# Optimization experiments

Hardware: AMD Instinct MI355X
Metric: run time of the kernel (lower is better)

## Reference

```python
import jax, jax.numpy as jnp
import numpy as np

HIDDEN = 1024
INTER = 4096
N_EXPERTS = 8
TOP_K = 2
INIT_STD = 0.02


def setup_inputs() -> dict:
    key = jax.random.key(0)
    ks = jax.random.split(key, 6)
    x = jax.random.normal(ks[0], (2, 1024, HIDDEN), dtype=jnp.float32)
    Wg = jax.random.normal(ks[1], (N_EXPERTS, HIDDEN), dtype=jnp.float32) * INIT_STD
    # Expert MLP params, stacked over experts. W1: [E, H, I], W2: [E, I, H].
    W1 = jax.random.normal(ks[2], (N_EXPERTS, HIDDEN, INTER), dtype=jnp.float32) * INIT_STD
    b1 = jnp.zeros((N_EXPERTS, INTER), dtype=jnp.float32)
    W2 = jax.random.normal(ks[3], (N_EXPERTS, INTER, HIDDEN), dtype=jnp.float32) * INIT_STD
    b2 = jnp.zeros((N_EXPERTS, HIDDEN), dtype=jnp.float32)
    return {"x": x, "Wg": Wg, "W1": W1, "b1": b1, "W2": W2, "b2": b2}


def reference(x, Wg, W1, b1, W2, b2):
    orig_shape = x.shape
    xt = x.reshape(-1, HIDDEN)              # [T, H]
    T = xt.shape[0]

    # Gating: top-k logits -> softmax over the k selected experts.
    logits = xt @ Wg.T                      # [T, E]
    topk_logits, topk_idx = jax.lax.top_k(logits, TOP_K)   # [T, K]
    w = jax.nn.softmax(topk_logits, axis=-1)               # [T, K]

    # Scatter top-k weights into a dense [T, E] gate matrix (zeros elsewhere).
    rows = jnp.arange(T)[:, None]
    gates = jnp.zeros((T, N_EXPERTS), xt.dtype).at[rows, topk_idx].add(w)

    # Dense expert compute (mathematically identical: non-selected experts get
    # gate weight 0). Expert MLP: Linear -> GELU (exact, erf) -> Linear.
    h = jnp.einsum('th,ehi->tei', xt, W1) + b1             # [T, E, I]
    h = jax.nn.gelu(h, approximate=False)
    o = jnp.einsum('tei,eih->teh', h, W2) + b2             # [T, E, H]
    y = jnp.einsum('te,teh->th', gates, o)                 # [T, H]
    return y.reshape(orig_shape)
```

## Files before the change

### kernel.cpp

```cpp
#include <hip/hip_runtime.h>
#include <hip/hip_bf16.h>

#define HID 1024
#define INTER 4096
#define NE 8
#define NTOK 2048
#define MAXROWS 5120

typedef __attribute__((ext_vector_type(8))) short short8v;
typedef __attribute__((ext_vector_type(4))) short short4v;
typedef __attribute__((ext_vector_type(4))) float f32x4;

__device__ __forceinline__ unsigned short f2bf(float f) {
  unsigned int u = __builtin_bit_cast(unsigned int, f);
  u = (u + 0x7FFFu + ((u >> 16) & 1u)) >> 16;
  return (unsigned short)u;
}
__device__ __forceinline__ float bf2f(unsigned short s) {
  unsigned int u = ((unsigned int)s) << 16;
  return __builtin_bit_cast(float, u);
}

typedef const __attribute__((address_space(1))) unsigned int* gas_t;
typedef __attribute__((address_space(3))) unsigned int* las_t;
__device__ __forceinline__ void gld16(const unsigned short* g, unsigned short* l) {
  __builtin_amdgcn_global_load_lds((gas_t)(const void*)g, (las_t)(void*)l, 16, 0, 0);
}

__device__ __forceinline__ void tconv_tile(const float* __restrict__ in,
                                           unsigned short* __restrict__ out,
                                           int R, int C, int bx, int by, int z,
                                           float* __restrict__ t) {
  const int r0 = by * 64, c0 = bx * 64;
  const int tr = threadIdx.x / 16;
  const int tc = (threadIdx.x % 16) * 4;
  const float* ip = in + ((size_t)z * R + r0) * (size_t)C + c0;
#pragma unroll
  for (int p = 0; p < 4; ++p) {
    f32x4 v = *(const f32x4*)&ip[(size_t)(p * 16 + tr) * C + tc];
    t[(p * 16 + tr) * 65 + tc + 0] = v[0];
    t[(p * 16 + tr) * 65 + tc + 1] = v[1];
    t[(p * 16 + tr) * 65 + tc + 2] = v[2];
    t[(p * 16 + tr) * 65 + tc + 3] = v[3];
  }
  __syncthreads();
  unsigned short* op = out + ((size_t)z * C + c0) * (size_t)R + r0;
#pragma unroll
  for (int p = 0; p < 4; ++p) {
    int c = p * 16 + tr;
    unsigned int a0 = (unsigned int)f2bf(t[(tc + 0) * 65 + c]) |
                      ((unsigned int)f2bf(t[(tc + 1) * 65 + c]) << 16);
    unsigned int a1 = (unsigned int)f2bf(t[(tc + 2) * 65 + c]) |
                      ((unsigned int)f2bf(t[(tc + 3) * 65 + c]) << 16);
    uint2 val; val.x = a0; val.y = a1;
    *(uint2*)&op[(size_t)c * R + tc] = val;
  }
}

__global__ __launch_bounds__(256) void prep_kernel(const float* __restrict__ x,
                                                   const float* __restrict__ W1,
                                                   const float* __restrict__ wg,
                                                   unsigned short* __restrict__ xb,
                                                   unsigned short* __restrict__ w1t,
                                                   int* __restrict__ tok_e,
                                                   float* __restrict__ tok_w) {
  __shared__ float sh[64 * 65];
  int bid = blockIdx.x;
  if (bid < 2048) {
    size_t i = (size_t)bid * 256 + threadIdx.x;
    f32x4 v = *(const f32x4*)&x[i * 4];
    uint2 r;
    r.x = (unsigned int)f2bf(v[0]) | ((unsigned int)f2bf(v[1]) << 16);
    r.y = (unsigned int)f2bf(v[2]) | ((unsigned int)f2bf(v[3]) << 16);
    *(uint2*)&xb[i * 4] = r;
    return;
  }
  bid -= 2048;
  if (bid < 8192) {
    tconv_tile(W1, w1t, HID, INTER, bid % 64, (bid / 64) % 16, bid / 1024, sh);
    return;
  }
  bid -= 8192;
  {
    const int t = bid;
    float acc[NE];
#pragma unroll
    for (int e = 0; e < NE; ++e) acc[e] = 0.f;
    for (int k = threadIdx.x; k < HID; k += 256) {
      float xv = x[(size_t)t * HID + k];
#pragma unroll
      for (int e = 0; e < NE; ++e) acc[e] += xv * wg[e * HID + k];
    }
#pragma unroll
    for (int e = 0; e < NE; ++e) {
#pragma unroll
      for (int off = 32; off >= 1; off >>= 1) acc[e] += __shfl_xor(acc[e], off, 64);
    }
    float* red = sh;
    const int wave = threadIdx.x >> 6, lane = threadIdx.x & 63;
    if (lane == 0) {
#pragma unroll
      for (int e = 0; e < NE; ++e) red[wave * NE + e] = acc[e];
    }
    __syncthreads();
    if (threadIdx.x == 0) {
      float l[NE];
#pragma unroll
      for (int e = 0; e < NE; ++e)
        l[e] = red[0 * NE + e] + red[1 * NE + e] + red[2 * NE + e] + red[3 * NE + e];
      int i0 = 0;
#pragma unroll
      for (int e = 1; e < NE; ++e) if (l[e] > l[i0]) i0 = e;
      int i1 = -1;
#pragma unroll
      for (int e = 0; e < NE; ++e) {
        if (e == i0) continue;
        if (i1 < 0 || l[e] > l[i1]) i1 = e;
      }
      float e1 = __expf(l[i1] - l[i0]);
      float w0 = 1.f / (1.f + e1);
      tok_e[t * 2 + 0] = i0;
      tok_e[t * 2 + 1] = i1;
      tok_w[t * 2 + 0] = w0;
      tok_w[t * 2 + 1] = 1.f - w0;
    }
  }
}

__global__ __launch_bounds__(512) void routing_kernel(const int* __restrict__ tok_e,
                                                      int* __restrict__ list_tok,
                                                      int* __restrict__ tok_gslot,
                                                      int* __restrict__ offs_out) {
  __shared__ int cnts[NE];
  __shared__ int offs_s[NE + 1];
  const int e = threadIdx.x >> 6, lane = threadIdx.x & 63;
  int c = 0;
  for (int base = 0; base < NTOK; base += 64) {
    int tok = base + lane;
    int e0 = tok_e[tok * 2], e1 = tok_e[tok * 2 + 1];
    bool m = (e0 == e) || (e1 == e);
    unsigned long long mask = __ballot(m);
    c += __popcll(mask);
  }
  if (lane == 0) cnts[e] = c;
  __syncthreads();
  if (threadIdx.x == 0) {
    int o = 0;
    for (int i = 0; i < NE; ++i) { offs_s[i] = o; o += (cnts[i] + 127) & ~127; }
    offs_s[NE] = o;
    for (int i = 0; i <= NE; ++i) offs_out[i] = offs_s[i];
  }
  __syncthreads();
  const int off = offs_s[e];
  int run = 0;
  for (int base = 0; base < NTOK; base += 64) {
    int tok = base + lane;
    int e0 = tok_e[tok * 2], e1 = tok_e[tok * 2 + 1];
    bool m = (e0 == e) || (e1 == e);
    unsigned long long mask = __ballot(m);
    int pos = run + __popcll(mask & ((1ull << lane) - 1ull));
    if (m) {
      int gs = off + pos;
      list_tok[gs] = tok;
      tok_gslot[tok * 2 + ((e0 == e) ? 0 : 1)] = gs;
    }
    run += __popcll(mask);
  }
  const int cnt = cnts[e];
  const int padded = (cnt + 127) & ~127;
  for (int p = cnt + lane; p < padded; p += 64) list_tok[off + p] = 0;
}

template <int KTOT, int NTOT, bool FIRST, int NSPLIT, int TCONVN>
__global__ __launch_bounds__(256, 3) void moe_gemm(const unsigned short* __restrict__ Abase,
                                                   const unsigned short* __restrict__ Bbase,
                                                   const float* __restrict__ bias,
                                                   const int* __restrict__ list_tok,
                                                   const int* __restrict__ offs,
                                                   void* __restrict__ outp,
                                                   const float* __restrict__ W2f,
                                                   unsigned short* __restrict__ w2t) {
  constexpr int KS = KTOT / NSPLIT;
  constexpr int NT = KS / 32;
  static_assert(NT >= 8 && (NT - 2) % 6 == 0, "NT must be 6k+2");
  constexpr int nM = MAXROWS / 128;
  constexpr int nN = NTOT / 128;
  constexpr int NWG_GEMM = nN * nM * NSPLIT;
  __shared__ __align__(16) unsigned short lds[3][2][4096];

  if (TCONVN != 0 && blockIdx.x >= NWG_GEMM) {
    int t = blockIdx.x - NWG_GEMM;
    tconv_tile(W2f, w2t, INTER, HID, t % 16, (t / 16) % 64, t / 1024,
               (float*)&lds[0][0][0]);
    return;
  }

  int wg = blockIdx.x;
  wg = (wg & 7) * (NWG_GEMM >> 3) + (wg >> 3);
  const int ks = (NSPLIT > 1) ? (wg / (nM * nN)) : 0;
  const int rem = wg % (nM * nN);
  const int mt = rem % nM;
  const int nt = rem / nM;
  const int grow0 = mt * 128;
  if (grow0 >= offs[NE]) return;
  int e = 0;
#pragma unroll
  for (int i = 1; i < NE; ++i) if (grow0 >= offs[i]) e = i;
  const int n0 = nt * 128;
  const int k0 = ks * KS;

  const int tid = threadIdx.x;
  const int wave = tid >> 6, lane = tid & 63;

  const int srow = tid >> 2;
  const int skc = (((tid & 3) ^ ((srow >> 1) & 3)) * 8);
  const unsigned short* ag[2];
  const unsigned short* bg[2];
#pragma unroll
  for (int j = 0; j < 2; ++j) {
    const int row = srow + j * 64;
    size_t arow;
    if (FIRST) arow = (size_t)list_tok[grow0 + row] * KTOT;
    else       arow = (size_t)(grow0 + row) * KTOT;
    ag[j] = Abase + arow + k0 + skc;
    bg[j] = Bbase + (size_t)e * NTOT * KTOT + (size_t)(n0 + row) * KTOT + k0 + skc;
  }
  const int wbase = wave * 512;

  const int wm = wave >> 1, wn = wave & 1;
  const int fr = lane & 15;
  const int q = lane >> 4;
  int aoff[4], boff[4];
#pragma unroll
  for (int m = 0; m < 4; ++m) {
    const int row = wm * 64 + m * 16 + fr;
    aoff[m] = row * 32 + ((q ^ ((row >> 1) & 3)) * 8);
  }
#pragma unroll
  for (int n = 0; n < 4; ++n) {
    const int row = wn * 64 + n * 16 + fr;
    boff[n] = row * 32 + ((q ^ ((row >> 1) & 3)) * 8);
  }

  f32x4 acc[4][4] = {};
  short8v af[2][4], bf[2][4];

#define STAGE(S, SLOT)                                             \
  {                                                                \
    gld16(ag[0] + (S) * 32, &lds[SLOT][0][wbase]);                 \
    gld16(ag[1] + (S) * 32, &lds[SLOT][0][wbase + 2048]);          \
    gld16(bg[0] + (S) * 32, &lds[SLOT][1][wbase]);                 \
    gld16(bg[1] + (S) * 32, &lds[SLOT][1][wbase + 2048]);          \
  }

#define READF(BK, SLN)                                                          \
  {                                                                             \
    _Pragma("unroll")                                                           \
    for (int m = 0; m < 4; ++m) af[BK][m] = *(const short8v*)&lds[SLN][0][aoff[m]]; \
    _Pragma("unroll")                                                           \
    for (int n = 0; n < 4; ++n) bf[BK][n] = *(const short8v*)&lds[SLN][1][boff[n]]; \
  }

#define MFMAC(BK)                                                  \
  {                                                                \
    __builtin_amdgcn_s_setprio(1);                                 \
    _Pragma("unroll")                                              \
    for (int n = 0; n < 4; ++n)                                    \
      _Pragma("unroll")                                            \
      for (int m = 0; m < 4; ++m)                                  \
        acc[m][n] = __builtin_amdgcn_mfma_f32_16x16x32_bf16(af[BK][m], bf[BK][n], acc[m][n], 0, 0, 0); \
    __builtin_amdgcn_s_setprio(0);                                 \
  }

#define ITER(S, SL, CUR, DOSTAGE, VMSTR)                           \
  {                                                                \
    if (DOSTAGE) STAGE((S) + 2, (((SL) + 2) % 3));                 \
    asm volatile("s_waitcnt vmcnt(" VMSTR ")" ::: "memory");       \
    asm volatile("s_barrier" ::: "memory");                        \
    __builtin_amdgcn_sched_barrier(0);                             \
    READF(1 - (CUR), (((SL) + 1) % 3));                            \
    __builtin_amdgcn_sched_barrier(0);                             \
    MFMAC(CUR);                                                    \
  }

  STAGE(0, 0);
  STAGE(1, 1);
  asm volatile("s_waitcnt vmcnt(4)" ::: "memory");
  asm volatile("s_barrier" ::: "memory");
  __builtin_amdgcn_sched_barrier(0);
  READF(0, 0);
  __builtin_amdgcn_sched_barrier(0);

  for (int s = 0; s < NT - 2; s += 6) {
    ITER(s + 0, 0, 0, true, "4");
    ITER(s + 1, 1, 1, true, "4");
    ITER(s + 2, 2, 0, true, "4");
    ITER(s + 3, 0, 1, true, "4");
    ITER(s + 4, 1, 0, true, "4");
    ITER(s + 5, 2, 1, true, "4");
  }
  ITER(NT - 2, 0, 0, false, "0");
  MFMAC(1);

#undef ITER
#undef MFMAC
#undef READF
#undef STAGE

  const int r4 = lane >> 4;
#pragma unroll
  for (int m = 0; m < 4; ++m) {
#pragma unroll
    for (int n = 0; n < 4; ++n) {
      const int gcol = n0 + wn * 64 + n * 16 + fr;
      float bv = 0.f;
      if (FIRST) bv = bias[e * NTOT + gcol];
#pragma unroll
      for (int r = 0; r < 4; ++r) {
        const int grow = grow0 + wm * 64 + m * 16 + r4 * 4 + r;
        float v = acc[m][n][r] + bv;
        if (FIRST) {
          v = 0.5f * v * (1.0f + erff(v * 0.70710678118654752f));
          ((unsigned short*)outp)[(size_t)grow * NTOT + gcol] = f2bf(v);
        } else {
          ((unsigned short*)outp)[((size_t)ks * MAXROWS + grow) * NTOT + gcol] = f2bf(v);
        }
      }
    }
  }
}

template <int NSPLIT>
__global__ __launch_bounds__(256) void combine_kernel(const unsigned short* __restrict__ part,
                                                      const int* __restrict__ tok_gslot,
                                                      const int* __restrict__ tok_e,
                                                      const float* __restrict__ tok_w,
                                                      const float* __restrict__ b2,
                                                      float* __restrict__ y) {
  const int t = blockIdx.x;
  const int c = threadIdx.x * 4;
  const int gs0 = tok_gslot[t * 2 + 0], gs1 = tok_gslot[t * 2 + 1];
  const int e0 = tok_e[t * 2 + 0], e1 = tok_e[t * 2 + 1];
  const float w0 = tok_w[t * 2 + 0], w1 = tok_w[t * 2 + 1];
  float s0[4] = {0.f, 0.f, 0.f, 0.f}, s1[4] = {0.f, 0.f, 0.f, 0.f};
#pragma unroll
  for (int ks = 0; ks < NSPLIT; ++ks) {
    short4v p0 = *(const short4v*)&part[((size_t)ks * MAXROWS + gs0) * HID + c];
    short4v p1 = *(const short4v*)&part[((size_t)ks * MAXROWS + gs1) * HID + c];
#pragma unroll
    for (int i = 0; i < 4; ++i) {
      s0[i] += bf2f((unsigned short)p0[i]);
      s1[i] += bf2f((unsigned short)p1[i]);
    }
  }
  f32x4 bb0 = *(const f32x4*)&b2[e0 * HID + c];
  f32x4 bb1 = *(const f32x4*)&b2[e1 * HID + c];
  f32x4 r;
#pragma unroll
  for (int i = 0; i < 4; ++i)
    r[i] = w0 * (s0[i] + bb0[i]) + w1 * (s1[i] + bb1[i]);
  *(f32x4*)&y[(size_t)t * HID + c] = r;
}

extern "C" void kernel_launch(void* const* d_in, const int* in_sizes, int n_in,
                              void* d_out, int out_size, void* d_ws, size_t ws_size,
                              hipStream_t stream) {
  const float* x  = (const float*)d_in[0];
  const float* wg = (const float*)d_in[1];
  const float* W1 = (const float*)d_in[2];
  const float* b1 = (const float*)d_in[3];
  const float* W2 = (const float*)d_in[4];
  const float* b2 = (const float*)d_in[5];
  float* y = (float*)d_out;

  unsigned char* ws = (unsigned char*)d_ws;
  size_t off = 0;
  unsigned short* w1t  = (unsigned short*)(ws + off);
  unsigned short* part = (unsigned short*)(ws + off); off += (size_t)NE * HID * INTER * 2;
  unsigned short* w2t  = (unsigned short*)(ws + off); off += (size_t)NE * INTER * HID * 2;
  unsigned short* xb   = (unsigned short*)(ws + off); off += (size_t)NTOK * HID * 2;
  unsigned short* h    = (unsigned short*)(ws + off); off += (size_t)MAXROWS * INTER * 2;
  int* tok_e           = (int*)(ws + off);            off += NTOK * 2 * 4;
  float* tok_w         = (float*)(ws + off);          off += NTOK * 2 * 4;
  int* tok_gslot       = (int*)(ws + off);            off += NTOK * 2 * 4;
  int* list_tok        = (int*)(ws + off);            off += MAXROWS * 4;
  int* offs            = (int*)(ws + off);            off += 64;
  (void)ws_size; (void)in_sizes; (void)n_in; (void)out_size;

  prep_kernel<<<2048 + 8192 + 2048, 256, 0, stream>>>(x, W1, wg, xb, w1t, tok_e, tok_w);
  routing_kernel<<<1, 512, 0, stream>>>(tok_e, list_tok, tok_gslot, offs);
  moe_gemm<HID, INTER, true, 1, 8192>
      <<<(INTER / 128) * (MAXROWS / 128) + 8192, 256, 0, stream>>>(
          xb, w1t, b1, list_tok, offs, (void*)h, W2, w2t);
  moe_gemm<INTER, HID, false, 4, 0>
      <<<(HID / 128) * (MAXROWS / 128) * 4, 256, 0, stream>>>(
          h, w2t, b2, list_tok, offs, (void*)part, nullptr, nullptr);
  combine_kernel<4><<<NTOK, 256, 0, stream>>>(part, tok_gslot, tok_e, tok_w, b2, y);
}
```

Measured before the change: 216.7 us.

## Read fp32 expert weights directly in GEMM, dropping separate transpose-convert passes

Removes the W1/W2 transpose-to-bf16 preprocessing tiles and instead has each GEMM workgroup load fp32 weight rows into registers, convert them with packed bf16 instructions, and write them transposed into LDS. A register double-buffer for B plus the existing triple-buffered async A staging make up a new pipeline schedule. This avoids writing and re-reading 64 MB of bf16 weight copies. The cost is that each B tile is loaded as fp32 (twice the bytes) once per M-tile, and conversion and LDS stores now sit inside the GEMM loop.

```diff
diff --git a/kernel.cpp b/kernel.cpp
--- a/kernel.cpp
+++ b/kernel.cpp
@@ -10,6 +10,8 @@
 typedef __attribute__((ext_vector_type(8))) short short8v;
 typedef __attribute__((ext_vector_type(4))) short short4v;
 typedef __attribute__((ext_vector_type(4))) float f32x4;
+typedef __attribute__((ext_vector_type(2))) float f32x2;
+typedef __attribute__((ext_vector_type(4))) unsigned int u32x4;
 
 __device__ __forceinline__ unsigned short f2bf(float f) {
   unsigned int u = __builtin_bit_cast(unsigned int, f);
@@ -27,44 +29,12 @@
   __builtin_amdgcn_global_load_lds((gas_t)(const void*)g, (las_t)(void*)l, 16, 0, 0);
 }
 
-__device__ __forceinline__ void tconv_tile(const float* __restrict__ in,
-                                           unsigned short* __restrict__ out,
-                                           int R, int C, int bx, int by, int z,
-                                           float* __restrict__ t) {
-  const int r0 = by * 64, c0 = bx * 64;
-  const int tr = threadIdx.x / 16;
-  const int tc = (threadIdx.x % 16) * 4;
-  const float* ip = in + ((size_t)z * R + r0) * (size_t)C + c0;
-#pragma unroll
-  for (int p = 0; p < 4; ++p) {
-    f32x4 v = *(const f32x4*)&ip[(size_t)(p * 16 + tr) * C + tc];
-    t[(p * 16 + tr) * 65 + tc + 0] = v[0];
-    t[(p * 16 + tr) * 65 + tc + 1] = v[1];
-    t[(p * 16 + tr) * 65 + tc + 2] = v[2];
-    t[(p * 16 + tr) * 65 + tc + 3] = v[3];
-  }
-  __syncthreads();
-  unsigned short* op = out + ((size_t)z * C + c0) * (size_t)R + r0;
-#pragma unroll
-  for (int p = 0; p < 4; ++p) {
-    int c = p * 16 + tr;
-    unsigned int a0 = (unsigned int)f2bf(t[(tc + 0) * 65 + c]) |
-                      ((unsigned int)f2bf(t[(tc + 1) * 65 + c]) << 16);
-    unsigned int a1 = (unsigned int)f2bf(t[(tc + 2) * 65 + c]) |
-                      ((unsigned int)f2bf(t[(tc + 3) * 65 + c]) << 16);
-    uint2 val; val.x = a0; val.y = a1;
-    *(uint2*)&op[(size_t)c * R + tc] = val;
-  }
-}
-
 __global__ __launch_bounds__(256) void prep_kernel(const float* __restrict__ x,
-                                                   const float* __restrict__ W1,
                                                    const float* __restrict__ wg,
                                                    unsigned short* __restrict__ xb,
-                                                   unsigned short* __restrict__ w1t,
                                                    int* __restrict__ tok_e,
                                                    float* __restrict__ tok_w) {
-  __shared__ float sh[64 * 65];
+  __shared__ float red[4 * NE];
   int bid = blockIdx.x;
   if (bid < 2048) {
     size_t i = (size_t)bid * 256 + threadIdx.x;
@@ -76,11 +46,6 @@
     return;
   }
   bid -= 2048;
-  if (bid < 8192) {
-    tconv_tile(W1, w1t, HID, INTER, bid % 64, (bid / 64) % 16, bid / 1024, sh);
-    return;
-  }
-  bid -= 8192;
   {
     const int t = bid;
     float acc[NE];
@@ -96,7 +61,6 @@
 #pragma unroll
       for (int off = 32; off >= 1; off >>= 1) acc[e] += __shfl_xor(acc[e], off, 64);
     }
-    float* red = sh;
     const int wave = threadIdx.x >> 6, lane = threadIdx.x & 63;
     if (lane == 0) {
 #pragma unroll
@@ -171,32 +135,26 @@
   for (int p = cnt + lane; p < padded; p += 64) list_tok[off + p] = 0;
 }
 
-template <int KTOT, int NTOT, bool FIRST, int NSPLIT, int TCONVN>
-__global__ __launch_bounds__(256, 3) void moe_gemm(const unsigned short* __restrict__ Abase,
-                                                   const unsigned short* __restrict__ Bbase,
-                                                   const float* __restrict__ bias,
-                                                   const int* __restrict__ list_tok,
-                                                   const int* __restrict__ offs,
-                                                   void* __restrict__ outp,
-                                                   const float* __restrict__ W2f,
-                                                   unsigned short* __restrict__ w2t) {
+template <int KTOT, int NTOT, bool FIRST, int NSPLIT>
+__global__ __launch_bounds__(256, 3) void moe_gemm_direct(
+    const unsigned short* __restrict__ Abase,
+    const float* __restrict__ Bf32,
+    const float* __restrict__ bias,
+    const int* __restrict__ list_tok,
+    const int* __restrict__ offs,
+    void* __restrict__ outp) {
   constexpr int KS = KTOT / NSPLIT;
   constexpr int NT = KS / 32;
   static_assert(NT >= 8 && (NT - 2) % 6 == 0, "NT must be 6k+2");
   constexpr int nM = MAXROWS / 128;
   constexpr int nN = NTOT / 128;
-  constexpr int NWG_GEMM = nN * nM * NSPLIT;
-  __shared__ __align__(16) unsigned short lds[3][2][4096];
-
-  if (TCONVN != 0 && blockIdx.x >= NWG_GEMM) {
-    int t = blockIdx.x - NWG_GEMM;
-    tconv_tile(W2f, w2t, INTER, HID, t % 16, (t / 16) % 64, t / 1024,
-               (float*)&lds[0][0][0]);
-    return;
-  }
+  constexpr int NWG = nN * nM * NSPLIT;
+
+  __shared__ __align__(16) unsigned short ldsA[3][4096];
+  __shared__ __align__(16) unsigned short ldsB[2][4096];
 
   int wg = blockIdx.x;
-  wg = (wg & 7) * (NWG_GEMM >> 3) + (wg >> 3);
+  wg = (wg & 7) * (NWG >> 3) + (wg >> 3);
   const int ks = (NSPLIT > 1) ? (wg / (nM * nN)) : 0;
   const int rem = wg % (nM * nN);
   const int mt = rem % nM;
@@ -215,7 +173,6 @@
   const int srow = tid >> 2;
   const int skc = (((tid & 3) ^ ((srow >> 1) & 3)) * 8);
   const unsigned short* ag[2];
-  const unsigned short* bg[2];
 #pragma unroll
   for (int j = 0; j < 2; ++j) {
     const int row = srow + j * 64;
@@ -223,9 +180,14 @@
     if (FIRST) arow = (size_t)list_tok[grow0 + row] * KTOT;
     else       arow = (size_t)(grow0 + row) * KTOT;
     ag[j] = Abase + arow + k0 + skc;
-    bg[j] = Bbase + (size_t)e * NTOT * KTOT + (size_t)(n0 + row) * KTOT + k0 + skc;
   }
   const int wbase = wave * 512;
+
+  const int kb = wave;
+  const int ncol = lane * 2;
+  const float* bsrc = Bf32 + (size_t)e * KTOT * NTOT
+                    + (size_t)(k0 + kb * 8) * NTOT + n0 + ncol;
+  const int bws = ncol * 32 + ((kb ^ ((ncol >> 1) & 3)) * 8);
 
   const int wm = wave >> 1, wn = wave & 1;
   const int fr = lane & 15;
@@ -243,69 +205,92 @@
   }
 
   f32x4 acc[4][4] = {};
-  short8v af[2][4], bf[2][4];
-
-#define STAGE(S, SLOT)                                             \
-  {                                                                \
-    gld16(ag[0] + (S) * 32, &lds[SLOT][0][wbase]);                 \
-    gld16(ag[1] + (S) * 32, &lds[SLOT][0][wbase + 2048]);          \
-    gld16(bg[0] + (S) * 32, &lds[SLOT][1][wbase]);                 \
-    gld16(bg[1] + (S) * 32, &lds[SLOT][1][wbase + 2048]);          \
-  }
-
-#define READF(BK, SLN)                                                          \
-  {                                                                             \
-    _Pragma("unroll")                                                           \
-    for (int m = 0; m < 4; ++m) af[BK][m] = *(const short8v*)&lds[SLN][0][aoff[m]]; \
-    _Pragma("unroll")                                                           \
-    for (int n = 0; n < 4; ++n) bf[BK][n] = *(const short8v*)&lds[SLN][1][boff[n]]; \
-  }
-
-#define MFMAC(BK)                                                  \
+  f32x2 breg0[8], breg1[8];
+
+#define ASTAGE(S, SLOT)                                            \
+  {                                                                \
+    gld16(ag[0] + (S) * 32, &ldsA[SLOT][wbase]);                   \
+    gld16(ag[1] + (S) * 32, &ldsA[SLOT][wbase + 2048]);            \
+  }
+
+#define BLOAD(S, R)                                                \
+  {                                                                \
+    _Pragma("unroll")                                              \
+    for (int j = 0; j < 8; ++j)                                    \
+      R[j] = *(const f32x2*)&bsrc[((size_t)((S) * 32 + j)) * NTOT]; \
+  }
+
+#define BWRITE(R, BUF)                                             \
+  {                                                                \
+    u32x4 vx, vy;                                                  \
+    _Pragma("unroll")                                              \
+    for (int j = 0; j < 4; ++j) {                                  \
+      unsigned int wx, wy;                                         \
+      asm("v_cvt_pk_bf16_f32 %0, %1, %2"                           \
+          : "=v"(wx) : "v"(R[2 * j][0]), "v"(R[2 * j + 1][0]));    \
+      asm("v_cvt_pk_bf16_f32 %0, %1, %2"                           \
+          : "=v"(wy) : "v"(R[2 * j][1]), "v"(R[2 * j + 1][1]));    \
+      vx[j] = wx; vy[j] = wy;                                      \
+    }                                                              \
+    *(u32x4*)&ldsB[BUF][bws] = vx;                                 \
+    *(u32x4*)&ldsB[BUF][bws + 32] = vy;                            \
+  }
+
+#define BSEL(P) ((P) ? breg1 : breg0)
+
+#define MFMAS()                                                    \
   {                                                                \
     __builtin_amdgcn_s_setprio(1);                                 \
     _Pragma("unroll")                                              \
     for (int n = 0; n < 4; ++n)                                    \
       _Pragma("unroll")                                            \
       for (int m = 0; m < 4; ++m)                                  \
-        acc[m][n] = __builtin_amdgcn_mfma_f32_16x16x32_bf16(af[BK][m], bf[BK][n], acc[m][n], 0, 0, 0); \
+        acc[m][n] = __builtin_amdgcn_mfma_f32_16x16x32_bf16(af[m], bf[n], acc[m][n], 0, 0, 0); \
     __builtin_amdgcn_s_setprio(0);                                 \
   }
 
-#define ITER(S, SL, CUR, DOSTAGE, VMSTR)                           \
-  {                                                                \
-    if (DOSTAGE) STAGE((S) + 2, (((SL) + 2) % 3));                 \
-    asm volatile("s_waitcnt vmcnt(" VMSTR ")" ::: "memory");       \
+#define ITER(S, SL, PAR, DOA, DOBW, DOBL, LKSTR)                   \
+  {                                                                \
+    short8v af[4], bf[4];                                          \
+    _Pragma("unroll")                                              \
+    for (int m = 0; m < 4; ++m) af[m] = *(const short8v*)&ldsA[SL][aoff[m]]; \
+    _Pragma("unroll")                                              \
+    for (int n = 0; n < 4; ++n) bf[n] = *(const short8v*)&ldsB[PAR][boff[n]]; \
+    if (DOA) ASTAGE((S) + 2, ((SL) + 2) % 3);                      \
+    if (DOBW) BWRITE(BSEL((PAR) ^ 1), (PAR) ^ 1);                  \
+    if (DOBL) BLOAD((S) + 2, BSEL(PAR));                           \
+    asm volatile("s_waitcnt lgkmcnt(" LKSTR ")" ::: "memory");     \
+    __builtin_amdgcn_sched_barrier(0);                             \
+    MFMAS();                                                       \
+    asm volatile("s_waitcnt lgkmcnt(0)" ::: "memory");             \
     asm volatile("s_barrier" ::: "memory");                        \
-    __builtin_amdgcn_sched_barrier(0);                             \
-    READF(1 - (CUR), (((SL) + 1) % 3));                            \
-    __builtin_amdgcn_sched_barrier(0);                             \
-    MFMAC(CUR);                                                    \
-  }
-
-  STAGE(0, 0);
-  STAGE(1, 1);
-  asm volatile("s_waitcnt vmcnt(4)" ::: "memory");
+  }
+
+  ASTAGE(0, 0);
+  ASTAGE(1, 1);
+  BLOAD(0, breg0);
+  BWRITE(breg0, 0);
+  BLOAD(1, breg1);
+  asm volatile("s_waitcnt lgkmcnt(0)" ::: "memory");
   asm volatile("s_barrier" ::: "memory");
-  __builtin_amdgcn_sched_barrier(0);
-  READF(0, 0);
-  __builtin_amdgcn_sched_barrier(0);
 
   for (int s = 0; s < NT - 2; s += 6) {
-    ITER(s + 0, 0, 0, true, "4");
-    ITER(s + 1, 1, 1, true, "4");
-    ITER(s + 2, 2, 0, true, "4");
-    ITER(s + 3, 0, 1, true, "4");
-    ITER(s + 4, 1, 0, true, "4");
-    ITER(s + 5, 2, 1, true, "4");
-  }
-  ITER(NT - 2, 0, 0, false, "0");
-  MFMAC(1);
+    ITER(s + 0, 0, 0, 1, 1, 1, "2");
+    ITER(s + 1, 1, 1, 1, 1, 1, "2");
+    ITER(s + 2, 2, 0, 1, 1, 1, "2");
+    ITER(s + 3, 0, 1, 1, 1, 1, "2");
+    ITER(s + 4, 1, 0, 1, 1, 1, "2");
+    ITER(s + 5, 2, 1, 1, 1, 1, "2");
+  }
+  ITER(NT - 2, 0, 0, 0, 1, 0, "2");
+  ITER(NT - 1, 1, 1, 0, 0, 0, "0");
 
 #undef ITER
-#undef MFMAC
-#undef READF
-#undef STAGE
+#undef MFMAS
+#undef BSEL
+#undef BWRITE
+#undef BLOAD
+#undef ASTAGE
 
   const int r4 = lane >> 4;
 #pragma unroll
@@ -375,11 +360,9 @@
 
   unsigned char* ws = (unsigned char*)d_ws;
   size_t off = 0;
-  unsigned short* w1t  = (unsigned short*)(ws + off);
-  unsigned short* part = (unsigned short*)(ws + off); off += (size_t)NE * HID * INTER * 2;
-  unsigned short* w2t  = (unsigned short*)(ws + off); off += (size_t)NE * INTER * HID * 2;
   unsigned short* xb   = (unsigned short*)(ws + off); off += (size_t)NTOK * HID * 2;
   unsigned short* h    = (unsigned short*)(ws + off); off += (size_t)MAXROWS * INTER * 2;
+  unsigned short* part = (unsigned short*)(ws + off); off += (size_t)4 * MAXROWS * HID * 2;
   int* tok_e           = (int*)(ws + off);            off += NTOK * 2 * 4;
   float* tok_w         = (float*)(ws + off);          off += NTOK * 2 * 4;
   int* tok_gslot       = (int*)(ws + off);            off += NTOK * 2 * 4;
@@ -387,13 +370,13 @@
   int* offs            = (int*)(ws + off);            off += 64;
   (void)ws_size; (void)in_sizes; (void)n_in; (void)out_size;
 
-  prep_kernel<<<2048 + 8192 + 2048, 256, 0, stream>>>(x, W1, wg, xb, w1t, tok_e, tok_w);
+  prep_kernel<<<2048 + 2048, 256, 0, stream>>>(x, wg, xb, tok_e, tok_w);
   routing_kernel<<<1, 512, 0, stream>>>(tok_e, list_tok, tok_gslot, offs);
-  moe_gemm<HID, INTER, true, 1, 8192>
-      <<<(INTER / 128) * (MAXROWS / 128) + 8192, 256, 0, stream>>>(
-          xb, w1t, b1, list_tok, offs, (void*)h, W2, w2t);
-  moe_gemm<INTER, HID, false, 4, 0>
+  moe_gemm_direct<HID, INTER, true, 1>
+      <<<(INTER / 128) * (MAXROWS / 128), 256, 0, stream>>>(
+          xb, W1, b1, list_tok, offs, (void*)h);
+  moe_gemm_direct<INTER, HID, false, 4>
       <<<(HID / 128) * (MAXROWS / 128) * 4, 256, 0, stream>>>(
-          h, w2t, b2, list_tok, offs, (void*)part, nullptr, nullptr);
+          h, W2, b2, list_tok, offs, (void*)part);
   combine_kernel<4><<<NTOK, 256, 0, stream>>>(part, tok_gslot, tok_e, tok_w, b2, y);
 }
```

Measured after the change: 220.9 us. No clear change (+1.9%).
